# Kernel optimization log

Hardware: AMD Instinct MI355X
Metric: run time of the kernel (lower is better)

Reference implementation:

```python
import jax, jax.numpy as jnp
import numpy as np

KEY_BITS = 3
VAL_BITS = 4
KEY_CLIP = 3.0  # fixed symmetric codebook range for per-dim key MSE quantizer


def setup_inputs() -> dict:
    key = jax.random.key(0)
    k1, k2, k3, k4 = jax.random.split(key, 4)
    B, H, Sq, Skv, D = 2, 32, 8, 4096, 128
    return {
        "query": jax.random.normal(k1, (B, H, Sq, D), dtype=jnp.float32),
        "keys": jax.random.normal(k2, (B, H, Skv, D), dtype=jnp.float32),
        "values": jax.random.normal(k3, (B, H, Skv, D), dtype=jnp.float32),
        "proj": jax.random.normal(k4, (D, D), dtype=jnp.float32),  # QJL projection S
    }


def _quantize_keys(keys, proj):
    # Per-dimension MSE quantization with fixed uniform codebook over [-A, A]
    L = 2 ** KEY_BITS
    A = KEY_CLIP
    step = 2.0 * A / (L - 1)
    idx = jnp.clip(jnp.round((keys + A) / step), 0, L - 1)  # mse_indices
    k_hat = idx * step - A
    resid = keys - k_hat
    res_norm = jnp.linalg.norm(resid, axis=-1, keepdims=True)  # (B,H,S,1)
    signs = jnp.sign(resid @ proj)  # qjl_signs, (B,H,S,m)
    return k_hat, signs, res_norm


def _dequantize_values(values):
    # ScalarValueQuantizer: per-token min/max uniform quant + dequant
    L = 2 ** VAL_BITS
    v_min = jnp.min(values, axis=-1, keepdims=True)
    v_max = jnp.max(values, axis=-1, keepdims=True)
    v_range = jnp.clip(v_max - v_min, 1e-8, None)
    idx = jnp.clip(jnp.round((values - v_min) / v_range * (L - 1)), 0, L - 1)
    return v_min + idx / (L - 1) * (v_max - v_min)


def reference(query, keys, values, proj):
    D = query.shape[-1]
    m = proj.shape[1]
    scale = 1.0 / jnp.sqrt(jnp.asarray(D, dtype=query.dtype))

    k_hat, signs, res_norm = _quantize_keys(keys, proj)

    # TurboQuant asymmetric score estimate: exact part + QJL residual estimate
    scores = jnp.einsum("bhqd,bhkd->bhqk", query, k_hat)
    qp = query @ proj  # (B,H,Sq,m)
    qjl_coef = jnp.sqrt(jnp.pi / 2.0).astype(query.dtype) / m
    scores = scores + qjl_coef * jnp.einsum("bhqm,bhkm->bhqk", qp, signs) * res_norm[..., 0][:, :, None, :]

    attn = jax.nn.softmax(scores * scale, axis=-1)  # (B,H,Sq,Skv)
    v_hat = _dequantize_values(values)
    return attn @ v_hat  # (B,H,Sq,D)
```

## Files before the change

### kernel.cpp

```cpp
#include <hip/hip_runtime.h>
#include <math.h>

#define NH     64
#define SQ     8
#define SKV    4096
#define DD     128
#define MM     128
#define CHUNK  256
#define NCHUNK (SKV / CHUNK)

#define OFF_QPT   0
#define OFF_PROJT (OFF_QPT + NH*MM*SQ)
#define OFF_O     (OFF_PROJT + MM*DD)
#define OFF_M     (OFF_O + NH*NCHUNK*SQ*DD)
#define OFF_L     (OFF_M + NH*NCHUNK*SQ)

__global__ __launch_bounds__(256) void k_prep(const float* __restrict__ query,
                                              const float* __restrict__ proj,
                                              float* __restrict__ ws) {
  float* qpT   = ws + OFF_QPT;
  float* projT = ws + OFF_PROJT;
  int b = blockIdx.x;
  if (b < NH) {
    __shared__ float qs[SQ * DD];
    const float* qrow = query + (size_t)b * SQ * DD;
    for (int i = threadIdx.x; i < SQ * DD; i += 256) qs[i] = qrow[i];
    __syncthreads();
    int j  = threadIdx.x & (MM - 1);
    int qh = threadIdx.x >> 7;
    float a0 = 0.f, a1 = 0.f, a2 = 0.f, a3 = 0.f;
    for (int d = 0; d < DD; ++d) {
      float pv = proj[d * MM + j];
      a0 += qs[(qh + 0) * DD + d] * pv;
      a1 += qs[(qh + 2) * DD + d] * pv;
      a2 += qs[(qh + 4) * DD + d] * pv;
      a3 += qs[(qh + 6) * DD + d] * pv;
    }
    float* dst = qpT + ((size_t)b * MM + j) * SQ;
    dst[qh + 0] = a0; dst[qh + 2] = a1; dst[qh + 4] = a2; dst[qh + 6] = a3;
  } else {
    int g = (b - NH) * 256 + threadIdx.x;
    int j = g >> 7, d = g & (DD - 1);
    projT[j * DD + d] = proj[d * MM + j];
  }
}

__global__ __launch_bounds__(256) void k_attn(const float* __restrict__ keys,
                                              const float* __restrict__ values,
                                              const float* __restrict__ query,
                                              float* ws) {
  const float* qpT_g   = ws + OFF_QPT;
  const float* projT_g = ws + OFF_PROJT;
  float* o_part = ws + OFF_O;
  float* m_part = ws + OFF_M;
  float* l_part = ws + OFF_L;

  __shared__ float qs[SQ * DD];
  __shared__ float qps[MM * SQ];
  __shared__ float vstat[CHUNK][2];
  union SmemU {
    float projT_h[64 * DD];
    struct {
      float p[CHUNK][SQ];
      float red[4][SQ];
      float oacc[4][SQ][DD];
    } ph2;
  };
  __shared__ SmemU u;

  const int tid  = threadIdx.x;
  const int lane = tid & 63;
  const int w    = tid >> 6;
  const int c    = blockIdx.x;
  const int h    = blockIdx.y;

  {
    const float4* s1 = (const float4*)(query + (size_t)h * SQ * DD);
    ((float4*)qs)[tid] = s1[tid];
    const float4* s2 = (const float4*)(qpT_g + (size_t)h * MM * SQ);
    ((float4*)qps)[tid] = s2[tid];
    const float4* s3 = (const float4*)projT_g;
    float4* d3 = (float4*)u.projT_h;
    #pragma unroll
    for (int i = 0; i < 8; ++i) d3[tid + i * 256] = s3[tid + i * 256];
  }
  __syncthreads();

  const int key = c * CHUNK + tid;
  const float* krow = keys + ((size_t)h * SKV + key) * DD;
  const float step = 6.0f / 7.0f;

  float resid[DD];
  float a[SQ];
  #pragma unroll
  for (int q = 0; q < SQ; ++q) a[q] = 0.f;
  float res2 = 0.f;

  #pragma unroll
  for (int d4 = 0; d4 < DD / 4; ++d4) {
    float4 kv = ((const float4*)krow)[d4];
    float kk[4] = {kv.x, kv.y, kv.z, kv.w};
    float kh[4];
    #pragma unroll
    for (int e = 0; e < 4; ++e) {
      float t  = (kk[e] + 3.0f) / step;
      float fi = fminf(fmaxf(rintf(t), 0.0f), 7.0f);
      kh[e] = fi * step - 3.0f;
      float r = kk[e] - kh[e];
      resid[d4 * 4 + e] = r;
      res2 += r * r;
    }
    #pragma unroll
    for (int q = 0; q < SQ; ++q) {
      float4 q4 = *(const float4*)(qs + q * DD + d4 * 4);
      a[q] += q4.x * kh[0]; a[q] += q4.y * kh[1];
      a[q] += q4.z * kh[2]; a[q] += q4.w * kh[3];
    }
  }

  {
    const float4* vrow = (const float4*)(values + ((size_t)h * SKV + key) * DD);
    float mn0 = 1e30f, mn1 = 1e30f, mx0 = -1e30f, mx1 = -1e30f;
    #pragma unroll 4
    for (int i = 0; i < DD / 4; ++i) {
      float4 vv = vrow[i];
      mn0 = fminf(mn0, fminf(vv.x, vv.y));
      mn1 = fminf(mn1, fminf(vv.z, vv.w));
      mx0 = fmaxf(mx0, fmaxf(vv.x, vv.y));
      mx1 = fmaxf(mx1, fmaxf(vv.z, vv.w));
    }
    vstat[tid][0] = fminf(mn0, mn1);
    vstat[tid][1] = fmaxf(mx0, mx1);
  }

  float y[SQ];
  #pragma unroll
  for (int q = 0; q < SQ; ++q) y[q] = 0.f;

  #pragma unroll 1
  for (int half = 0; half < 2; ++half) {
    if (half == 1) {
      __syncthreads();
      const float4* src = (const float4*)(projT_g + 64 * DD);
      float4* dst = (float4*)u.projT_h;
      #pragma unroll
      for (int i = 0; i < 8; ++i) dst[tid + i * 256] = src[tid + i * 256];
      __syncthreads();
    }
    #pragma unroll 1
    for (int mmi = 0; mmi < 64; ++mmi) {
      const float4* prow = (const float4*)(u.projT_h + mmi * DD);
      float z0 = 0.f, z1 = 0.f, z2 = 0.f, z3 = 0.f;
      #pragma unroll
      for (int d4 = 0; d4 < DD / 4; ++d4) {
        float4 pv = prow[d4];
        z0 += resid[4 * d4 + 0] * pv.x;
        z1 += resid[4 * d4 + 1] * pv.y;
        z2 += resid[4 * d4 + 2] * pv.z;
        z3 += resid[4 * d4 + 3] * pv.w;
      }
      float z = (z0 + z1) + (z2 + z3);
      float s = (z > 0.f) ? 1.f : ((z < 0.f) ? -1.f : 0.f);
      const int m = half * 64 + mmi;
      const float4* qpm = (const float4*)(qps + m * SQ);
      float4 pa = qpm[0], pb = qpm[1];
      y[0] += s * pa.x; y[1] += s * pa.y; y[2] += s * pa.z; y[3] += s * pa.w;
      y[4] += s * pb.x; y[5] += s * pb.y; y[6] += s * pb.z; y[7] += s * pb.w;
    }
  }

  const float qjl_coef = sqrtf(1.5707964f) * 0.0078125f;
  const float scale    = 1.0f / sqrtf(128.0f);
  const float rn = sqrtf(res2);
  float sc[SQ];
  #pragma unroll
  for (int q = 0; q < SQ; ++q) sc[q] = (a[q] + qjl_coef * y[q] * rn) * scale;

  float wred[SQ];
  #pragma unroll
  for (int q = 0; q < SQ; ++q) {
    float v = sc[q];
    #pragma unroll
    for (int off = 32; off > 0; off >>= 1) v = fmaxf(v, __shfl_xor(v, off));
    wred[q] = v;
  }
  __syncthreads();
  if (lane == 0) {
    #pragma unroll
    for (int q = 0; q < SQ; ++q) u.ph2.red[w][q] = wred[q];
  }
  __syncthreads();
  float p[SQ];
  #pragma unroll
  for (int q = 0; q < SQ; ++q) {
    float M = fmaxf(fmaxf(u.ph2.red[0][q], u.ph2.red[1][q]),
                    fmaxf(u.ph2.red[2][q], u.ph2.red[3][q]));
    p[q] = expf(sc[q] - M);
    u.ph2.p[tid][q] = p[q];
  }
  if (tid < SQ) {
    float M = fmaxf(fmaxf(u.ph2.red[0][tid], u.ph2.red[1][tid]),
                    fmaxf(u.ph2.red[2][tid], u.ph2.red[3][tid]));
    m_part[((size_t)h * NCHUNK + c) * SQ + tid] = M;
  }
  #pragma unroll
  for (int q = 0; q < SQ; ++q) {
    float v = p[q];
    #pragma unroll
    for (int off = 32; off > 0; off >>= 1) v += __shfl_xor(v, off);
    wred[q] = v;
  }
  __syncthreads();
  if (lane == 0) {
    #pragma unroll
    for (int q = 0; q < SQ; ++q) u.ph2.red[w][q] = wred[q];
  }
  __syncthreads();
  if (tid < SQ) {
    l_part[((size_t)h * NCHUNK + c) * SQ + tid] =
        u.ph2.red[0][tid] + u.ph2.red[1][tid] +
        u.ph2.red[2][tid] + u.ph2.red[3][tid];
  }

  float o[SQ][2];
  #pragma unroll
  for (int q = 0; q < SQ; ++q) { o[q][0] = 0.f; o[q][1] = 0.f; }
  const int d0 = 2 * lane;
  const float inv15 = 1.0f / 15.0f;
  #pragma unroll 1
  for (int kk = 0; kk < 64; ++kk) {
    const int kl = w * 64 + kk;
    const float2 vv = *(const float2*)(values + ((size_t)h * SKV + c * CHUNK + kl) * DD + d0);
    const float vmn = vstat[kl][0], vmx = vstat[kl][1];
    const float vr  = fmaxf(vmx - vmn, 1e-8f);
    float t0 = (vv.x - vmn) / vr * 15.0f;
    float t1 = (vv.y - vmn) / vr * 15.0f;
    float i0 = fminf(fmaxf(rintf(t0), 0.f), 15.f);
    float i1 = fminf(fmaxf(rintf(t1), 0.f), 15.f);
    float vh0 = vmn + i0 * inv15 * (vmx - vmn);
    float vh1 = vmn + i1 * inv15 * (vmx - vmn);
    const float4* pk = (const float4*)(&u.ph2.p[kl][0]);
    float4 pa = pk[0], pb = pk[1];
    o[0][0] += pa.x * vh0; o[0][1] += pa.x * vh1;
    o[1][0] += pa.y * vh0; o[1][1] += pa.y * vh1;
    o[2][0] += pa.z * vh0; o[2][1] += pa.z * vh1;
    o[3][0] += pa.w * vh0; o[3][1] += pa.w * vh1;
    o[4][0] += pb.x * vh0; o[4][1] += pb.x * vh1;
    o[5][0] += pb.y * vh0; o[5][1] += pb.y * vh1;
    o[6][0] += pb.z * vh0; o[6][1] += pb.z * vh1;
    o[7][0] += pb.w * vh0; o[7][1] += pb.w * vh1;
  }
  #pragma unroll
  for (int q = 0; q < SQ; ++q) {
    u.ph2.oacc[w][q][d0]     = o[q][0];
    u.ph2.oacc[w][q][d0 + 1] = o[q][1];
  }
  __syncthreads();
  for (int i = tid; i < SQ * DD; i += 256) {
    int q = i >> 7, d = i & (DD - 1);
    float vsum = u.ph2.oacc[0][q][d] + u.ph2.oacc[1][q][d] +
                 u.ph2.oacc[2][q][d] + u.ph2.oacc[3][q][d];
    o_part[(((size_t)h * NCHUNK + c) * SQ + q) * DD + d] = vsum;
  }
}

__global__ __launch_bounds__(128) void k_comb(const float* __restrict__ ws,
                                              float* __restrict__ out) {
  const float* o_part = ws + OFF_O;
  const float* m_part = ws + OFF_M;
  const float* l_part = ws + OFF_L;
  int hq = blockIdx.x;
  int h = hq >> 3, q = hq & 7;
  int d = threadIdx.x;
  float M = -1e30f;
  for (int cc = 0; cc < NCHUNK; ++cc)
    M = fmaxf(M, m_part[((size_t)h * NCHUNK + cc) * SQ + q]);
  float L = 0.f, acc = 0.f;
  for (int cc = 0; cc < NCHUNK; ++cc) {
    float mw = expf(m_part[((size_t)h * NCHUNK + cc) * SQ + q] - M);
    L   += mw * l_part[((size_t)h * NCHUNK + cc) * SQ + q];
    acc += mw * o_part[(((size_t)h * NCHUNK + cc) * SQ + q) * DD + d];
  }
  out[(size_t)hq * DD + d] = acc / L;
}

extern "C" void kernel_launch(void* const* d_in, const int* in_sizes, int n_in,
                              void* d_out, int out_size, void* d_ws, size_t ws_size,
                              hipStream_t stream) {
  const float* query  = (const float*)d_in[0];
  const float* keys   = (const float*)d_in[1];
  const float* values = (const float*)d_in[2];
  const float* proj   = (const float*)d_in[3];
  float* out = (float*)d_out;
  float* ws  = (float*)d_ws;

  k_prep<<<dim3(128), dim3(256), 0, stream>>>(query, proj, ws);
  k_attn<<<dim3(NCHUNK, NH), dim3(256), 0, stream>>>(keys, values, query, ws);
  k_comb<<<dim3(NH * SQ), dim3(128), 0, stream>>>(ws, out);
}
```

Before: 1.387 ms.

## Load full projection to LDS, compute value min/max via wave shuffles

Shared memory now holds the whole 128x128 projection, so the mid-loop barrier and reload of the second half are gone. The separate per-thread pass over each value row for min/max is removed; min/max is instead computed inside the PV loop with wave-wide shuffle reductions, which drops one full read of the values. Key quantization is split into blocks with scheduling barriers, and FMAs are made explicit. LDS use grows to about 64KB for projT plus 24KB for the other buffers, which may lower occupancy, and each PV iteration now carries 12 shuffles.

```diff
diff --git a/kernel.cpp b/kernel.cpp
--- a/kernel.cpp
+++ b/kernel.cpp
@@ -57,16 +57,10 @@
 
   __shared__ float qs[SQ * DD];
   __shared__ float qps[MM * SQ];
-  __shared__ float vstat[CHUNK][2];
-  union SmemU {
-    float projT_h[64 * DD];
-    struct {
-      float p[CHUNK][SQ];
-      float red[4][SQ];
-      float oacc[4][SQ][DD];
-    } ph2;
-  };
-  __shared__ SmemU u;
+  __shared__ float projT_s[MM * DD];
+  __shared__ float p_s[CHUNK][SQ];
+  __shared__ float red[4][SQ];
+  __shared__ float oacc[4][SQ][DD];
 
   const int tid  = threadIdx.x;
   const int lane = tid & 63;
@@ -80,14 +74,15 @@
     const float4* s2 = (const float4*)(qpT_g + (size_t)h * MM * SQ);
     ((float4*)qps)[tid] = s2[tid];
     const float4* s3 = (const float4*)projT_g;
-    float4* d3 = (float4*)u.projT_h;
-    #pragma unroll
-    for (int i = 0; i < 8; ++i) d3[tid + i * 256] = s3[tid + i * 256];
+    float4* d3 = (float4*)projT_s;
+    #pragma unroll
+    for (int i = 0; i < 16; ++i) d3[tid + i * 256] = s3[tid + i * 256];
   }
   __syncthreads();
 
   const int key = c * CHUNK + tid;
   const float* krow = keys + ((size_t)h * SKV + key) * DD;
+  const float4* kr4 = (const float4*)krow;
   const float step = 6.0f / 7.0f;
 
   float resid[DD];
@@ -96,77 +91,72 @@
   for (int q = 0; q < SQ; ++q) a[q] = 0.f;
   float res2 = 0.f;
 
-  #pragma unroll
-  for (int d4 = 0; d4 < DD / 4; ++d4) {
-    float4 kv = ((const float4*)krow)[d4];
-    float kk[4] = {kv.x, kv.y, kv.z, kv.w};
-    float kh[4];
-    #pragma unroll
-    for (int e = 0; e < 4; ++e) {
-      float t  = (kk[e] + 3.0f) / step;
-      float fi = fminf(fmaxf(rintf(t), 0.0f), 7.0f);
-      kh[e] = fi * step - 3.0f;
-      float r = kk[e] - kh[e];
-      resid[d4 * 4 + e] = r;
-      res2 += r * r;
-    }
-    #pragma unroll
-    for (int q = 0; q < SQ; ++q) {
-      float4 q4 = *(const float4*)(qs + q * DD + d4 * 4);
-      a[q] += q4.x * kh[0]; a[q] += q4.y * kh[1];
-      a[q] += q4.z * kh[2]; a[q] += q4.w * kh[3];
-    }
-  }
-
-  {
-    const float4* vrow = (const float4*)(values + ((size_t)h * SKV + key) * DD);
-    float mn0 = 1e30f, mn1 = 1e30f, mx0 = -1e30f, mx1 = -1e30f;
-    #pragma unroll 4
-    for (int i = 0; i < DD / 4; ++i) {
-      float4 vv = vrow[i];
-      mn0 = fminf(mn0, fminf(vv.x, vv.y));
-      mn1 = fminf(mn1, fminf(vv.z, vv.w));
-      mx0 = fmaxf(mx0, fmaxf(vv.x, vv.y));
-      mx1 = fmaxf(mx1, fmaxf(vv.z, vv.w));
-    }
-    vstat[tid][0] = fminf(mn0, mn1);
-    vstat[tid][1] = fmaxf(mx0, mx1);
-  }
+#define PA_BLOCK(Q0)                                                        \
+  _Pragma("unroll")                                                         \
+  for (int d4 = (Q0); d4 < (Q0) + 8; ++d4) {                                \
+    float4 kv = kr4[d4];                                                    \
+    float t0 = (kv.x + 3.0f) / step, t1 = (kv.y + 3.0f) / step;             \
+    float t2 = (kv.z + 3.0f) / step, t3 = (kv.w + 3.0f) / step;             \
+    float f0 = fminf(fmaxf(rintf(t0), 0.f), 7.f);                           \
+    float f1 = fminf(fmaxf(rintf(t1), 0.f), 7.f);                           \
+    float f2 = fminf(fmaxf(rintf(t2), 0.f), 7.f);                           \
+    float f3 = fminf(fmaxf(rintf(t3), 0.f), 7.f);                           \
+    float h0 = f0 * step - 3.0f, h1 = f1 * step - 3.0f;                     \
+    float h2 = f2 * step - 3.0f, h3 = f3 * step - 3.0f;                     \
+    float r0 = kv.x - h0, r1 = kv.y - h1, r2 = kv.z - h2, r3 = kv.w - h3;   \
+    resid[4 * d4 + 0] = r0; resid[4 * d4 + 1] = r1;                         \
+    resid[4 * d4 + 2] = r2; resid[4 * d4 + 3] = r3;                         \
+    res2 += r0 * r0; res2 += r1 * r1; res2 += r2 * r2; res2 += r3 * r3;     \
+    _Pragma("unroll")                                                       \
+    for (int q = 0; q < SQ; ++q) {                                          \
+      float4 q4 = *(const float4*)(qs + q * DD + 4 * d4);                   \
+      a[q] = fmaf(q4.x, h0, fmaf(q4.y, h1, fmaf(q4.z, h2,                   \
+             fmaf(q4.w, h3, a[q]))));                                       \
+    }                                                                       \
+  }
+
+  PA_BLOCK(0)
+  __builtin_amdgcn_sched_barrier(0);
+  PA_BLOCK(8)
+  __builtin_amdgcn_sched_barrier(0);
+  PA_BLOCK(16)
+  __builtin_amdgcn_sched_barrier(0);
+  PA_BLOCK(24)
+  __builtin_amdgcn_sched_barrier(0);
 
   float y[SQ];
   #pragma unroll
   for (int q = 0; q < SQ; ++q) y[q] = 0.f;
 
   #pragma unroll 1
-  for (int half = 0; half < 2; ++half) {
-    if (half == 1) {
-      __syncthreads();
-      const float4* src = (const float4*)(projT_g + 64 * DD);
-      float4* dst = (float4*)u.projT_h;
-      #pragma unroll
-      for (int i = 0; i < 8; ++i) dst[tid + i * 256] = src[tid + i * 256];
-      __syncthreads();
-    }
-    #pragma unroll 1
-    for (int mmi = 0; mmi < 64; ++mmi) {
-      const float4* prow = (const float4*)(u.projT_h + mmi * DD);
-      float z0 = 0.f, z1 = 0.f, z2 = 0.f, z3 = 0.f;
-      #pragma unroll
-      for (int d4 = 0; d4 < DD / 4; ++d4) {
-        float4 pv = prow[d4];
-        z0 += resid[4 * d4 + 0] * pv.x;
-        z1 += resid[4 * d4 + 1] * pv.y;
-        z2 += resid[4 * d4 + 2] * pv.z;
-        z3 += resid[4 * d4 + 3] * pv.w;
-      }
-      float z = (z0 + z1) + (z2 + z3);
-      float s = (z > 0.f) ? 1.f : ((z < 0.f) ? -1.f : 0.f);
-      const int m = half * 64 + mmi;
-      const float4* qpm = (const float4*)(qps + m * SQ);
-      float4 pa = qpm[0], pb = qpm[1];
-      y[0] += s * pa.x; y[1] += s * pa.y; y[2] += s * pa.z; y[3] += s * pa.w;
-      y[4] += s * pb.x; y[5] += s * pb.y; y[6] += s * pb.z; y[7] += s * pb.w;
-    }
+  for (int m = 0; m < MM; ++m) {
+    const float4* prow4 = (const float4*)(projT_s + m * DD);
+    float z0 = 0.f, z1 = 0.f, z2 = 0.f, z3 = 0.f;
+    #pragma unroll
+    for (int d4 = 0; d4 < 16; ++d4) {
+      float4 pv = prow4[d4];
+      z0 = fmaf(resid[4 * d4 + 0], pv.x, z0);
+      z1 = fmaf(resid[4 * d4 + 1], pv.y, z1);
+      z2 = fmaf(resid[4 * d4 + 2], pv.z, z2);
+      z3 = fmaf(resid[4 * d4 + 3], pv.w, z3);
+    }
+    __builtin_amdgcn_sched_barrier(0);
+    #pragma unroll
+    for (int d4 = 16; d4 < 32; ++d4) {
+      float4 pv = prow4[d4];
+      z0 = fmaf(resid[4 * d4 + 0], pv.x, z0);
+      z1 = fmaf(resid[4 * d4 + 1], pv.y, z1);
+      z2 = fmaf(resid[4 * d4 + 2], pv.z, z2);
+      z3 = fmaf(resid[4 * d4 + 3], pv.w, z3);
+    }
+    float zz = (z0 + z1) + (z2 + z3);
+    float s = (zz > 0.f) ? 1.f : ((zz < 0.f) ? -1.f : 0.f);
+    const float4* qpm = (const float4*)(qps + m * SQ);
+    float4 pa = qpm[0], pb = qpm[1];
+    y[0] = fmaf(s, pa.x, y[0]); y[1] = fmaf(s, pa.y, y[1]);
+    y[2] = fmaf(s, pa.z, y[2]); y[3] = fmaf(s, pa.w, y[3]);
+    y[4] = fmaf(s, pb.x, y[4]); y[5] = fmaf(s, pb.y, y[5]);
+    y[6] = fmaf(s, pb.z, y[6]); y[7] = fmaf(s, pb.w, y[7]);
   }
 
   const float qjl_coef = sqrtf(1.5707964f) * 0.0078125f;
@@ -184,23 +174,21 @@
     for (int off = 32; off > 0; off >>= 1) v = fmaxf(v, __shfl_xor(v, off));
     wred[q] = v;
   }
-  __syncthreads();
   if (lane == 0) {
     #pragma unroll
-    for (int q = 0; q < SQ; ++q) u.ph2.red[w][q] = wred[q];
+    for (int q = 0; q < SQ; ++q) red[w][q] = wred[q];
   }
   __syncthreads();
   float p[SQ];
   #pragma unroll
   for (int q = 0; q < SQ; ++q) {
-    float M = fmaxf(fmaxf(u.ph2.red[0][q], u.ph2.red[1][q]),
-                    fmaxf(u.ph2.red[2][q], u.ph2.red[3][q]));
+    float M = fmaxf(fmaxf(red[0][q], red[1][q]), fmaxf(red[2][q], red[3][q]));
     p[q] = expf(sc[q] - M);
-    u.ph2.p[tid][q] = p[q];
+    p_s[tid][q] = p[q];
   }
   if (tid < SQ) {
-    float M = fmaxf(fmaxf(u.ph2.red[0][tid], u.ph2.red[1][tid]),
-                    fmaxf(u.ph2.red[2][tid], u.ph2.red[3][tid]));
+    float M = fmaxf(fmaxf(red[0][tid], red[1][tid]),
+                    fmaxf(red[2][tid], red[3][tid]));
     m_part[((size_t)h * NCHUNK + c) * SQ + tid] = M;
   }
   #pragma unroll
@@ -213,13 +201,12 @@
   __syncthreads();
   if (lane == 0) {
     #pragma unroll
-    for (int q = 0; q < SQ; ++q) u.ph2.red[w][q] = wred[q];
+    for (int q = 0; q < SQ; ++q) red[w][q] = wred[q];
   }
   __syncthreads();
   if (tid < SQ) {
     l_part[((size_t)h * NCHUNK + c) * SQ + tid] =
-        u.ph2.red[0][tid] + u.ph2.red[1][tid] +
-        u.ph2.red[2][tid] + u.ph2.red[3][tid];
+        red[0][tid] + red[1][tid] + red[2][tid] + red[3][tid];
   }
 
   float o[SQ][2];
@@ -227,39 +214,45 @@
   for (int q = 0; q < SQ; ++q) { o[q][0] = 0.f; o[q][1] = 0.f; }
   const int d0 = 2 * lane;
   const float inv15 = 1.0f / 15.0f;
-  #pragma unroll 1
+  #pragma unroll 2
   for (int kk = 0; kk < 64; ++kk) {
     const int kl = w * 64 + kk;
-    const float2 vv = *(const float2*)(values + ((size_t)h * SKV + c * CHUNK + kl) * DD + d0);
-    const float vmn = vstat[kl][0], vmx = vstat[kl][1];
-    const float vr  = fmaxf(vmx - vmn, 1e-8f);
-    float t0 = (vv.x - vmn) / vr * 15.0f;
-    float t1 = (vv.y - vmn) / vr * 15.0f;
+    const float2 vv = *(const float2*)(values +
+        ((size_t)h * SKV + c * CHUNK + kl) * DD + d0);
+    float mn = fminf(vv.x, vv.y), mx = fmaxf(vv.x, vv.y);
+    #pragma unroll
+    for (int off = 32; off > 0; off >>= 1) {
+      mn = fminf(mn, __shfl_xor(mn, off));
+      mx = fmaxf(mx, __shfl_xor(mx, off));
+    }
+    const float vr = fmaxf(mx - mn, 1e-8f);
+    float t0 = (vv.x - mn) / vr * 15.0f;
+    float t1 = (vv.y - mn) / vr * 15.0f;
     float i0 = fminf(fmaxf(rintf(t0), 0.f), 15.f);
     float i1 = fminf(fmaxf(rintf(t1), 0.f), 15.f);
-    float vh0 = vmn + i0 * inv15 * (vmx - vmn);
-    float vh1 = vmn + i1 * inv15 * (vmx - vmn);
-    const float4* pk = (const float4*)(&u.ph2.p[kl][0]);
+    float vh0 = mn + i0 * inv15 * (mx - mn);
+    float vh1 = mn + i1 * inv15 * (mx - mn);
+    const float4* pk = (const float4*)(&p_s[kl][0]);
     float4 pa = pk[0], pb = pk[1];
-    o[0][0] += pa.x * vh0; o[0][1] += pa.x * vh1;
-    o[1][0] += pa.y * vh0; o[1][1] += pa.y * vh1;
-    o[2][0] += pa.z * vh0; o[2][1] += pa.z * vh1;
-    o[3][0] += pa.w * vh0; o[3][1] += pa.w * vh1;
-    o[4][0] += pb.x * vh0; o[4][1] += pb.x * vh1;
-    o[5][0] += pb.y * vh0; o[5][1] += pb.y * vh1;
-    o[6][0] += pb.z * vh0; o[6][1] += pb.z * vh1;
-    o[7][0] += pb.w * vh0; o[7][1] += pb.w * vh1;
-  }
-  #pragma unroll
-  for (int q = 0; q < SQ; ++q) {
-    u.ph2.oacc[w][q][d0]     = o[q][0];
-    u.ph2.oacc[w][q][d0 + 1] = o[q][1];
+    o[0][0] = fmaf(pa.x, vh0, o[0][0]); o[0][1] = fmaf(pa.x, vh1, o[0][1]);
+    o[1][0] = fmaf(pa.y, vh0, o[1][0]); o[1][1] = fmaf(pa.y, vh1, o[1][1]);
+    o[2][0] = fmaf(pa.z, vh0, o[2][0]); o[2][1] = fmaf(pa.z, vh1, o[2][1]);
+    o[3][0] = fmaf(pa.w, vh0, o[3][0]); o[3][1] = fmaf(pa.w, vh1, o[3][1]);
+    o[4][0] = fmaf(pb.x, vh0, o[4][0]); o[4][1] = fmaf(pb.x, vh1, o[4][1]);
+    o[5][0] = fmaf(pb.y, vh0, o[5][0]); o[5][1] = fmaf(pb.y, vh1, o[5][1]);
+    o[6][0] = fmaf(pb.z, vh0, o[6][0]); o[6][1] = fmaf(pb.z, vh1, o[6][1]);
+    o[7][0] = fmaf(pb.w, vh0, o[7][0]); o[7][1] = fmaf(pb.w, vh1, o[7][1]);
+  }
+  #pragma unroll
+  for (int q = 0; q < SQ; ++q) {
+    oacc[w][q][d0]     = o[q][0];
+    oacc[w][q][d0 + 1] = o[q][1];
   }
   __syncthreads();
   for (int i = tid; i < SQ * DD; i += 256) {
     int q = i >> 7, d = i & (DD - 1);
-    float vsum = u.ph2.oacc[0][q][d] + u.ph2.oacc[1][q][d] +
-                 u.ph2.oacc[2][q][d] + u.ph2.oacc[3][q][d];
+    float vsum = oacc[0][q][d] + oacc[1][q][d] +
+                 oacc[2][q][d] + oacc[3][q][d];
     o_part[(((size_t)h * NCHUNK + c) * SQ + q) * DD + d] = vsum;
   }
 }
```

After: 1.318 ms. 5.0% less time.
